# Kernel tuning notes

Measured on AMD Instinct MI355X. Metric: run time of the kernel, lower is better.

Reference implementation:

```python
import jax, jax.numpy as jnp
import numpy as np

N, A, B, H = 16, 2048, 2048, 64


def setup_inputs() -> dict:
    key = jax.random.key(0)
    k1, k2, k3, k4 = jax.random.split(key, 4)
    query = jax.random.normal(k1, (N, A, H), dtype=jnp.float32)
    key_t = jax.random.normal(k2, (N, B, H), dtype=jnp.float32)
    value = jax.random.normal(k3, (N, B, H), dtype=jnp.float32)
    mask = jax.random.randint(k4, (N, B), 0, 2).astype(bool)  # True = masked out
    return {"query": query, "key": key_t, "value": value, "mask": mask}


def reference(query, key, value, mask):
    # attention_product: scaled dot product -> (n, a, b) logits
    h = query.shape[-1]
    scale = 1.0 / jnp.sqrt(jnp.asarray(h, dtype=query.dtype))
    logit = jnp.einsum("nah,nbh->nab", query, key) * scale
    # mask (n, b) broadcast over query axis; masked positions -> -inf
    logit = jnp.where(mask[:, None, :], -jnp.inf, logit)
    attn = jax.nn.softmax(logit, axis=-1)
    # dropout_rate = 0.0 (eval) -> identity
    context = jnp.einsum("nab,nbh->nah", attn, value)
    return context
```

## Files before the change

kernel.cpp:

```cpp
#include <hip/hip_runtime.h>

#define NB 16
#define AQ 2048
#define BKV 2048
#define HD 64

#define QSCALE 0.18033688f
#define MBIAS -43000.0f

typedef float f32x4 __attribute__((ext_vector_type(4)));
typedef float f32x16 __attribute__((ext_vector_type(16)));
typedef short bf16x8 __attribute__((ext_vector_type(8)));
typedef int int4v __attribute__((ext_vector_type(4)));

__device__ __forceinline__ short f2bf(float f) {
  return __builtin_bit_cast(short, static_cast<__bf16>(f));
}
__device__ __forceinline__ unsigned pk2(float a, float b) {
  unsigned lo = (unsigned short)f2bf(a);
  unsigned hh = (unsigned short)f2bf(b);
  return lo | (hh << 16);
}

__global__ __launch_bounds__(256) void prepack(const float* __restrict__ K,
                                               const float* __restrict__ V,
                                               short* __restrict__ Kb,
                                               short* __restrict__ Vt) {
  if (blockIdx.x < 1024) {
    size_t base = ((size_t)blockIdx.x * 256 + threadIdx.x) * 8;
    f32x4 a = *(const f32x4*)(K + base);
    f32x4 b = *(const f32x4*)(K + base + 4);
    bf16x8 o;
#pragma unroll
    for (int i = 0; i < 4; ++i) {
      o[i] = f2bf(a[i]);
      o[i + 4] = f2bf(b[i]);
    }
    *(bf16x8*)(Kb + base) = o;
  } else {
    unsigned vb = blockIdx.x - 1024;
    int n = vb >> 5;
    int b0 = (vb & 31) * 64;
    int t = threadIdx.x;
    __shared__ short tile[64][68];
    int rb = t >> 4;
    int hc = (t & 15) * 4;
#pragma unroll
    for (int j = 0; j < 4; ++j) {
      int r = rb + 16 * j;
      f32x4 v = *(const f32x4*)(V + ((size_t)n * BKV + b0 + r) * HD + hc);
#pragma unroll
      for (int i = 0; i < 4; ++i) tile[r][hc + i] = f2bf(v[i]);
    }
    __syncthreads();
    int hr = t >> 2;
    int bb = (t & 3) * 16;
    bf16x8 o0, o1;
#pragma unroll
    for (int j = 0; j < 8; ++j) {
      o0[j] = tile[bb + j][hr];
      o1[j] = tile[bb + 8 + j][hr];
    }
    short* dst = Vt + ((size_t)n * HD + hr) * BKV + b0 + bb;
    *(bf16x8*)dst = o0;
    *(bf16x8*)(dst + 8) = o1;
  }
}

template <int PRE>
__global__ __launch_bounds__(256, 4) void attn_fwd(
    const float* __restrict__ Q, const float* __restrict__ K,
    const float* __restrict__ V, const int* __restrict__ M,
    const short* __restrict__ Kb, const short* __restrict__ Vt,
    float* __restrict__ O) {
  unsigned orig = blockIdx.x;
  unsigned wg = (orig & 7u) * 128u + (orig >> 3);
  int n = (int)(wg >> 6);
  int q0 = (int)(wg & 63u) * 32;

  int w = threadIdx.x >> 6;
  int lane = threadIdx.x & 63;
  int hi = lane >> 5;
  int li = lane & 31;

  const float* Qn = Q + (size_t)n * AQ * HD;
  const float* Kn = K + (size_t)n * BKV * HD;
  const float* Vn = V + (size_t)n * BKV * HD;
  const short* Kbn = Kb + (size_t)n * BKV * HD;
  const short* Vtn = Vt + (size_t)n * HD * BKV;
  const int* Mn = M + (size_t)n * BKV;

  __shared__ __align__(16) float pacc[4][32][68];
  __shared__ float Ml[4][2][32];

  bf16x8 qb[4];
#pragma unroll
  for (int ks = 0; ks < 4; ++ks) {
    const float* qp = Qn + (size_t)(q0 + li) * HD + 16 * ks + 8 * hi;
    f32x4 a = *(const f32x4*)qp;
    f32x4 b = *(const f32x4*)(qp + 4);
#pragma unroll
    for (int i = 0; i < 4; ++i) {
      qb[ks][i] = f2bf(a[i] * QSCALE);
      qb[ks][i + 4] = f2bf(b[i] * QSCALE);
    }
  }

  f32x16 acc0 = {};
  f32x16 acc1 = {};
  float m_run = -1e30f;
  float l_run = 0.f;

  const int bstart = w * (BKV / 4);
  for (int b0 = bstart; b0 < bstart + (BKV / 4); b0 += 32) {
    int4v mv[4];
#pragma unroll
    for (int j = 0; j < 4; ++j)
      mv[j] = *(const int4v*)(Mn + b0 + 8 * j + 4 * hi);
    f32x16 st;
#pragma unroll
    for (int j = 0; j < 4; ++j)
#pragma unroll
      for (int r = 0; r < 4; ++r) st[4 * j + r] = mv[j][r] ? MBIAS : 0.f;

#pragma unroll
    for (int ks = 0; ks < 4; ++ks) {
      bf16x8 ka;
      if constexpr (PRE) {
        ka = *(const bf16x8*)(Kbn + (size_t)(b0 + li) * HD + 16 * ks + 8 * hi);
      } else {
        const float* kp = Kn + (size_t)(b0 + li) * HD + 16 * ks + 8 * hi;
        f32x4 k0 = *(const f32x4*)kp;
        f32x4 k1 = *(const f32x4*)(kp + 4);
#pragma unroll
        for (int i = 0; i < 4; ++i) {
          ka[i] = f2bf(k0[i]);
          ka[i + 4] = f2bf(k1[i]);
        }
      }
      st = __builtin_amdgcn_mfma_f32_32x32x16_bf16(ka, qb[ks], st, 0, 0, 0);
    }

    float mt = st[0];
#pragma unroll
    for (int i = 1; i < 16; ++i) mt = fmaxf(mt, st[i]);
    mt = fmaxf(mt, __shfl_xor(mt, 32));
    float m_new = fmaxf(m_run, mt);
    float fac = exp2f(m_run - m_new);

    float rs = 0.f;
#pragma unroll
    for (int i = 0; i < 16; ++i) {
      float e = exp2f(st[i] - m_new);
      st[i] = e;
      rs += e;
    }
    rs += __shfl_xor(rs, 32);
    l_run = l_run * fac + rs;
    m_run = m_new;

#pragma unroll
    for (int i = 0; i < 16; ++i) {
      acc0[i] *= fac;
      acc1[i] *= fac;
    }

    unsigned w8[8], sx[8];
#pragma unroll
    for (int j = 0; j < 8; ++j) w8[j] = pk2(st[2 * j], st[2 * j + 1]);
#pragma unroll
    for (int j = 0; j < 8; ++j) sx[j] = (unsigned)__shfl_xor((int)w8[j], 32);
    int4v p0 = {(int)(hi ? sx[2] : w8[0]), (int)(hi ? sx[3] : w8[1]),
                (int)(hi ? w8[2] : sx[0]), (int)(hi ? w8[3] : sx[1])};
    int4v p1 = {(int)(hi ? sx[6] : w8[4]), (int)(hi ? sx[7] : w8[5]),
                (int)(hi ? w8[6] : sx[4]), (int)(hi ? w8[7] : sx[5])};
    bf16x8 pb0 = __builtin_bit_cast(bf16x8, p0);
    bf16x8 pb1 = __builtin_bit_cast(bf16x8, p1);

#pragma unroll
    for (int ht = 0; ht < 2; ++ht) {
      bf16x8 va0, va1;
      if constexpr (PRE) {
        const short* vp = Vtn + (size_t)(32 * ht + li) * BKV + b0 + 8 * hi;
        va0 = *(const bf16x8*)vp;
        va1 = *(const bf16x8*)(vp + 16);
      } else {
#pragma unroll
        for (int j = 0; j < 8; ++j) {
          va0[j] = f2bf(Vn[(size_t)(b0 + 8 * hi + j) * HD + 32 * ht + li]);
          va1[j] = f2bf(Vn[(size_t)(b0 + 16 + 8 * hi + j) * HD + 32 * ht + li]);
        }
      }
      if (ht == 0) {
        acc0 = __builtin_amdgcn_mfma_f32_32x32x16_bf16(va0, pb0, acc0, 0, 0, 0);
        acc0 = __builtin_amdgcn_mfma_f32_32x32x16_bf16(va1, pb1, acc0, 0, 0, 0);
      } else {
        acc1 = __builtin_amdgcn_mfma_f32_32x32x16_bf16(va0, pb0, acc1, 0, 0, 0);
        acc1 = __builtin_amdgcn_mfma_f32_32x32x16_bf16(va1, pb1, acc1, 0, 0, 0);
      }
    }
  }

  if (hi == 0) {
    Ml[w][0][li] = m_run;
    Ml[w][1][li] = l_run;
  }
#pragma unroll
  for (int reg = 0; reg < 16; ++reg) {
    int hrow = (reg & 3) + 8 * (reg >> 2) + 4 * hi;
    pacc[w][li][hrow] = acc0[reg];
    pacc[w][li][32 + hrow] = acc1[reg];
  }
  __syncthreads();

  {
    int tid = threadIdx.x;
    int q = tid >> 3;
    int hb = (tid & 7) * 8;
    float m0 = Ml[0][0][q], m1 = Ml[1][0][q];
    float m2 = Ml[2][0][q], m3 = Ml[3][0][q];
    float mmax = fmaxf(fmaxf(m0, m1), fmaxf(m2, m3));
    float f[4] = {exp2f(m0 - mmax), exp2f(m1 - mmax), exp2f(m2 - mmax),
                  exp2f(m3 - mmax)};
    float l = f[0] * Ml[0][1][q] + f[1] * Ml[1][1][q] + f[2] * Ml[2][1][q] +
              f[3] * Ml[3][1][q];
    float inv = 1.0f / l;
    float* op = O + ((size_t)n * AQ + q0 + q) * HD + hb;
#pragma unroll
    for (int t = 0; t < 2; ++t) {
      f32x4 o = {0.f, 0.f, 0.f, 0.f};
#pragma unroll
      for (int ww = 0; ww < 4; ++ww) {
        f32x4 a = *(const f32x4*)&pacc[ww][q][hb + 4 * t];
#pragma unroll
        for (int i = 0; i < 4; ++i) o[i] += f[ww] * a[i];
      }
      f32x4 res;
#pragma unroll
      for (int i = 0; i < 4; ++i) res[i] = o[i] * inv;
      *(f32x4*)(op + 4 * t) = res;
    }
  }
}

extern "C" void kernel_launch(void* const* d_in, const int* in_sizes, int n_in,
                              void* d_out, int out_size, void* d_ws, size_t ws_size,
                              hipStream_t stream) {
  const float* q = (const float*)d_in[0];
  const float* k = (const float*)d_in[1];
  const float* v = (const float*)d_in[2];
  const int* m = (const int*)d_in[3];
  float* o = (float*)d_out;

  const size_t kv_elems = (size_t)NB * BKV * HD;
  const size_t need = kv_elems * 2 * sizeof(short);

  if (ws_size >= need) {
    short* kb = (short*)d_ws;
    short* vt = kb + kv_elems;
    prepack<<<dim3(1536), dim3(256), 0, stream>>>(k, v, kb, vt);
    attn_fwd<1><<<dim3(NB * (AQ / 32)), dim3(256), 0, stream>>>(q, k, v, m, kb, vt, o);
  } else {
    attn_fwd<0><<<dim3(NB * (AQ / 32)), dim3(256), 0, stream>>>(q, k, v, m, nullptr, nullptr, o);
  }
}
```

Measured before the change: 148.6 us.

## Add lazy softmax rescale, permlane32 swap, setprio around MFMA, tree max

The online softmax now skips the running-max update and accumulator rescale unless some lane's new tile max exceeds the running max by more than a threshold. This is the FA4-style lazy rescaling and trades bounded exponent growth for fewer multiplies. The eight cross-half shuffles used to build the P operand are replaced by four permlane32_swap ops. s_setprio is raised around the MFMA blocks, and the row-max reduction becomes a shallower tree. Together these aim to cut VALU and cross-lane work in the inner loop, at the risk of larger intermediate values before final normalization.

```diff
diff --git a/kernel.cpp b/kernel.cpp
--- a/kernel.cpp
+++ b/kernel.cpp
@@ -7,6 +7,7 @@
 
 #define QSCALE 0.18033688f
 #define MBIAS -43000.0f
+#define DTHR 8.0f
 
 typedef float f32x4 __attribute__((ext_vector_type(4)));
 typedef float f32x16 __attribute__((ext_vector_type(16)));
@@ -123,6 +124,7 @@
 #pragma unroll
       for (int r = 0; r < 4; ++r) st[4 * j + r] = mv[j][r] ? MBIAS : 0.f;
 
+    __builtin_amdgcn_s_setprio(1);
 #pragma unroll
     for (int ks = 0; ks < 4; ++ks) {
       bf16x8 ka;
@@ -140,40 +142,49 @@
       }
       st = __builtin_amdgcn_mfma_f32_32x32x16_bf16(ka, qb[ks], st, 0, 0, 0);
     }
-
-    float mt = st[0];
-#pragma unroll
-    for (int i = 1; i < 16; ++i) mt = fmaxf(mt, st[i]);
+    __builtin_amdgcn_s_setprio(0);
+
+    float a0 = fmaxf(fmaxf(st[0], st[1]), st[2]);
+    float a1 = fmaxf(fmaxf(st[3], st[4]), st[5]);
+    float a2 = fmaxf(fmaxf(st[6], st[7]), st[8]);
+    float a3 = fmaxf(fmaxf(st[9], st[10]), st[11]);
+    float a4 = fmaxf(fmaxf(st[12], st[13]), st[14]);
+    float mt = fmaxf(fmaxf(fmaxf(a0, a1), fmaxf(a2, a3)), fmaxf(a4, st[15]));
     mt = fmaxf(mt, __shfl_xor(mt, 32));
-    float m_new = fmaxf(m_run, mt);
-    float fac = exp2f(m_run - m_new);
+
+    if (!__all(mt - m_run <= DTHR)) {
+      float m_new = fmaxf(m_run, mt);
+      float fac = exp2f(m_run - m_new);
+      l_run *= fac;
+#pragma unroll
+      for (int i = 0; i < 16; ++i) {
+        acc0[i] *= fac;
+        acc1[i] *= fac;
+      }
+      m_run = m_new;
+    }
 
     float rs = 0.f;
 #pragma unroll
     for (int i = 0; i < 16; ++i) {
-      float e = exp2f(st[i] - m_new);
+      float e = exp2f(st[i] - m_run);
       st[i] = e;
       rs += e;
     }
     rs += __shfl_xor(rs, 32);
-    l_run = l_run * fac + rs;
-    m_run = m_new;
-
-#pragma unroll
-    for (int i = 0; i < 16; ++i) {
-      acc0[i] *= fac;
-      acc1[i] *= fac;
-    }
-
-    unsigned w8[8], sx[8];
+    l_run += rs;
+
+    unsigned w8[8];
 #pragma unroll
     for (int j = 0; j < 8; ++j) w8[j] = pk2(st[2 * j], st[2 * j + 1]);
-#pragma unroll
-    for (int j = 0; j < 8; ++j) sx[j] = (unsigned)__shfl_xor((int)w8[j], 32);
-    int4v p0 = {(int)(hi ? sx[2] : w8[0]), (int)(hi ? sx[3] : w8[1]),
-                (int)(hi ? w8[2] : sx[0]), (int)(hi ? w8[3] : sx[1])};
-    int4v p1 = {(int)(hi ? sx[6] : w8[4]), (int)(hi ? sx[7] : w8[5]),
-                (int)(hi ? w8[6] : sx[4]), (int)(hi ? w8[7] : sx[5])};
+    auto s02 = __builtin_amdgcn_permlane32_swap((int)w8[0], (int)w8[2], false, false);
+    auto s13 = __builtin_amdgcn_permlane32_swap((int)w8[1], (int)w8[3], false, false);
+    auto s46 = __builtin_amdgcn_permlane32_swap((int)w8[4], (int)w8[6], false, false);
+    auto s57 = __builtin_amdgcn_permlane32_swap((int)w8[5], (int)w8[7], false, false);
+    int4v p0 = {static_cast<int>(s02[0]), static_cast<int>(s13[0]),
+                static_cast<int>(s02[1]), static_cast<int>(s13[1])};
+    int4v p1 = {static_cast<int>(s46[0]), static_cast<int>(s57[0]),
+                static_cast<int>(s46[1]), static_cast<int>(s57[1])};
     bf16x8 pb0 = __builtin_bit_cast(bf16x8, p0);
     bf16x8 pb1 = __builtin_bit_cast(bf16x8, p1);
 
@@ -191,6 +202,7 @@
           va1[j] = f2bf(Vn[(size_t)(b0 + 16 + 8 * hi + j) * HD + 32 * ht + li]);
         }
       }
+      __builtin_amdgcn_s_setprio(1);
       if (ht == 0) {
         acc0 = __builtin_amdgcn_mfma_f32_32x32x16_bf16(va0, pb0, acc0, 0, 0, 0);
         acc0 = __builtin_amdgcn_mfma_f32_32x32x16_bf16(va1, pb1, acc0, 0, 0, 0);
@@ -198,6 +210,7 @@
         acc1 = __builtin_amdgcn_mfma_f32_32x32x16_bf16(va0, pb0, acc1, 0, 0, 0);
         acc1 = __builtin_amdgcn_mfma_f32_32x32x16_bf16(va1, pb1, acc1, 0, 0, 0);
       }
+      __builtin_amdgcn_s_setprio(0);
     }
   }
 
```

New measurement: 147.6 us. Within noise of the previous version (-0.7%).
